# Kernel optimization log

Hardware: AMD Instinct MI355X
Metric: run time of the kernel (lower is better)

Reference implementation:

```python
import jax, jax.numpy as jnp
import numpy as np

N_NODES = 50000
N_EDGES = 500000
F_DIM = 128
N_REL = 8
N_LAYERS = 2
NEG_SLOPE = 0.2  # PyG RGATConv default negative_slope


def setup_inputs() -> dict:
    key = jax.random.key(0)
    ks = jax.random.split(key, 6)
    x = jax.random.normal(ks[0], (N_NODES, F_DIM), dtype=jnp.float32)
    edge_index = jax.random.randint(ks[1], (2, N_EDGES), 0, N_NODES)
    edge_type = jax.random.randint(ks[2], (N_EDGES,), 0, N_REL)
    # Per-layer relation weights [L, R, F_in, F_out], attention vectors q,k [L, F_out, 1], bias [L, F_out]
    W = jax.random.normal(ks[3], (N_LAYERS, N_REL, F_DIM, F_DIM), dtype=jnp.float32) * (1.0 / np.sqrt(F_DIM)).astype(np.float32)
    att_q = jax.random.normal(ks[4], (N_LAYERS, F_DIM, 1), dtype=jnp.float32) * 0.1
    att_k = jax.random.normal(ks[5], (N_LAYERS, F_DIM, 1), dtype=jnp.float32) * 0.1
    bias = jnp.zeros((N_LAYERS, F_DIM), dtype=jnp.float32)
    return {"x": x, "W": W, "att_q": att_q, "att_k": att_k, "bias": bias,
            "edge_index": edge_index, "edge_type": edge_type}


def _segment_softmax(logits, seg, num_segments):
    # Numerically stable softmax over edges grouped by destination node.
    m = jax.ops.segment_max(logits, seg, num_segments=num_segments)
    m = jax.lax.stop_gradient(m)
    e = jnp.exp(logits - m[seg])
    denom = jax.ops.segment_sum(e, seg, num_segments=num_segments)
    return e / (denom[seg] + 1e-16)


def _rgat_layer(h, src, dst, edge_type, W, q, k, b):
    # h: [N, F]; W: [R, F, F]. Project once per relation, then gather per edge
    # (avoids materializing [E, F, F] per-edge weight gathers).
    n = h.shape[0]
    xw = jnp.einsum('nf,rfg->rng', h, W)          # [R, N, F]
    out_j = xw[edge_type, src]                    # [E, F] transformed source feats
    out_i = xw[edge_type, dst]                    # [E, F] transformed dest feats
    # additive self-attention: leaky_relu(q(x_i) + k(x_j)), heads=1, dim=1
    logits = jax.nn.leaky_relu((out_i @ q + out_j @ k)[:, 0], NEG_SLOPE)  # [E]
    alpha = _segment_softmax(logits, dst, n)      # across-relation softmax per dst node
    agg = jax.ops.segment_sum(alpha[:, None] * out_j, dst, num_segments=n)  # [N, F]
    return agg + b


def reference(x, W, att_q, att_k, bias, edge_index, edge_type):
    src, dst = edge_index[0], edge_index[1]
    h = x
    for l in range(W.shape[0]):  # small fixed layer count
        h = _rgat_layer(h, src, dst, edge_type, W[l], att_q[l], att_k[l], bias[l])
        h = jax.nn.relu(h)  # dropout is identity in eval mode
    return h
```

## Files before the change

kernel.cpp:

```cpp
#include <hip/hip_runtime.h>
#include <hip/hip_bf16.h>
#include <hip/hip_fp16.h>

#define N_NODES 50000
#define N_EDGES 500000
#define F_DIM   128
#define N_REL   8
#define N_LAYERS 2
#define NEG_SLOPE 0.2f

#define NBLK_N ((N_NODES + 255) / 256)

typedef _Float16 half8 __attribute__((ext_vector_type(8)));
typedef float f32x4  __attribute__((ext_vector_type(4)));


__device__ inline float lrelu(float l) { return (l > 0.f) ? l : NEG_SLOPE * l; }

__global__ __launch_bounds__(256) void prep_h(const float* __restrict__ H,
                                              _Float16* __restrict__ Hf) {
    const size_t i8 = (size_t)blockIdx.x * 256 + threadIdx.x;
    if (i8 >= (size_t)N_NODES * F_DIM / 8) return;
    const float* src = H + i8 * 8;
    float av[8];
    *(float4*)(av)     = *(const float4*)(src);
    *(float4*)(av + 4) = *(const float4*)(src + 4);
    alignas(16) _Float16 hb[8];
#pragma unroll
    for (int j = 0; j < 8; ++j) hb[j] = (_Float16)av[j];
    *(uint4*)(Hf + i8 * 8) = *(const uint4*)hb;
}

__global__ __launch_bounds__(256) void prep_w(const float* __restrict__ W,
                                              _Float16* __restrict__ Wf) {
    __shared__ float tile[64][F_DIM + 1];
    const int mat = blockIdx.x;
    const float* src = W + (size_t)mat * F_DIM * F_DIM;
    const int t = threadIdx.x;
    for (int hf = 0; hf < 2; ++hf) {
#pragma unroll
        for (int i = 0; i < 8; ++i) {
            int idx = t + i * 256;
            int f = idx >> 5, c4 = idx & 31;
            float4 v = *(const float4*)(src + (size_t)(hf * 64 + f) * F_DIM + c4 * 4);
            *(float4*)&tile[f][c4 * 4] = v;
        }
        __syncthreads();
        int g = t >> 1, fs = (t & 1) * 32;
        for (int c = 0; c < 4; ++c) {
            alignas(16) _Float16 th[8];
#pragma unroll
            for (int j = 0; j < 8; ++j) th[j] = (_Float16)tile[fs + c * 8 + j][g];
            size_t o = ((size_t)mat * F_DIM + g) * F_DIM + hf * 64 + fs + c * 8;
            *(uint4*)(Wf + o) = *(const uint4*)th;
        }
        __syncthreads();
    }
}

#define GBM 128
#define RGRP 4
__global__ __launch_bounds__(256, 2) void gemm_xw(const _Float16* __restrict__ Hf,
                                                  const _Float16* __restrict__ Wf,
                                                  const float* __restrict__ qv_g,
                                                  const float* __restrict__ kv_g,
                                                  __half* __restrict__ xw,
                                                  float* __restrict__ a_q,
                                                  float* __restrict__ a_k) {
    __shared__ _Float16 lds[F_DIM * F_DIM];
    const int rb0 = blockIdx.x * GBM;
    const int r0  = blockIdx.y * RGRP;
    const int tid = threadIdx.x;
    const int lane = tid & 63, w = tid >> 6;
    const int q = lane >> 4, ln = lane & 15;

    half8 Af[2][4];
#pragma unroll
    for (int rt = 0; rt < 2; ++rt) {
        int row = rb0 + w * 32 + rt * 16 + ln;
        int ar = (row < N_NODES) ? row : (N_NODES - 1);
        const _Float16* hp = Hf + (size_t)ar * F_DIM;
#pragma unroll
        for (int ks = 0; ks < 4; ++ks)
            Af[rt][ks] = *(const half8*)(hp + ks * 32 + q * 8);
    }

    float qvl[8], kvl[8];
#pragma unroll
    for (int t = 0; t < 8; ++t) {
        qvl[t] = qv_g[t * 16 + ln];
        kvl[t] = kv_g[t * 16 + ln];
    }

    for (int rr = 0; rr < RGRP; ++rr) {
        const int r = r0 + rr;
        __syncthreads();
        {
            const _Float16* src = Wf + (size_t)r * F_DIM * F_DIM;
#pragma unroll
            for (int i = 0; i < 8; ++i) {
                int chunk = tid + i * 256;
                int gg = chunk >> 4, c8 = chunk & 15;
                uint4 v = *(const uint4*)(src + gg * F_DIM + c8 * 8);
                *(uint4*)(lds + gg * F_DIM + ((c8 ^ (gg & 15)) * 8)) = v;
            }
        }
        __syncthreads();

        f32x4 acc[2][8];
#pragma unroll
        for (int rt = 0; rt < 2; ++rt)
#pragma unroll
            for (int t = 0; t < 8; ++t) acc[rt][t] = (f32x4)(0.f);

#pragma unroll
        for (int ks = 0; ks < 4; ++ks) {
            const int jx = (((ks * 4 + q) ^ ln)) << 3;
            half8 Bf[8];
#pragma unroll
            for (int c = 0; c < 8; ++c)
                Bf[c] = *(const half8*)(lds + (c * 16 + ln) * F_DIM + jx);
#pragma unroll
            for (int c = 0; c < 8; ++c)
#pragma unroll
                for (int rt = 0; rt < 2; ++rt)
                    acc[rt][c] = __builtin_amdgcn_mfma_f32_16x16x32_f16(Af[rt][ks], Bf[c], acc[rt][c], 0, 0, 0);
        }

#pragma unroll
        for (int rt = 0; rt < 2; ++rt) {
            float pq[4], pk[4];
#pragma unroll
            for (int reg = 0; reg < 4; ++reg) {
                const int row = rb0 + w * 32 + rt * 16 + q * 4 + reg;
                alignas(16) unsigned short hs[8];
                float sq = 0.f, sk = 0.f;
#pragma unroll
                for (int t = 0; t < 8; ++t) {
                    float v = acc[rt][t][reg];
                    __half hv = __float2half(v);
                    hs[t] = *reinterpret_cast<unsigned short*>(&hv);
                    sq = fmaf(v, qvl[t], sq);
                    sk = fmaf(v, kvl[t], sk);
                }
                if (row < N_NODES)
                    *(uint4*)(xw + ((size_t)r * N_NODES + row) * F_DIM + ln * 8) = *(const uint4*)hs;
                pq[reg] = sq; pk[reg] = sk;
            }
#pragma unroll
            for (int reg = 0; reg < 4; ++reg) {
#pragma unroll
                for (int m = 1; m <= 8; m <<= 1) {
                    pq[reg] += __shfl_xor(pq[reg], m);
                    pk[reg] += __shfl_xor(pk[reg], m);
                }
            }
            if (ln == 0) {
#pragma unroll
                for (int reg = 0; reg < 4; ++reg) {
                    const int row = rb0 + w * 32 + rt * 16 + q * 4 + reg;
                    if (row < N_NODES) {
                        a_q[r * N_NODES + row] = pq[reg];
                        a_k[r * N_NODES + row] = pk[reg];
                    }
                }
            }
        }
    }
}


__global__ __launch_bounds__(256) void count_kernel(const int* __restrict__ dstp,
                                                    int* __restrict__ cnt) {
    int e = blockIdx.x * 256 + threadIdx.x;
    if (e < N_EDGES) atomicAdd(cnt + dstp[e], 1);
}

__global__ __launch_bounds__(256) void block_sum_kernel(const int* __restrict__ cnt,
                                                        int* __restrict__ partial) {
    __shared__ int s[256];
    int idx = blockIdx.x * 256 + threadIdx.x;
    int v = (idx < N_NODES) ? cnt[idx] : 0;
    s[threadIdx.x] = v;
    __syncthreads();
    for (int off = 128; off > 0; off >>= 1) {
        if (threadIdx.x < off) s[threadIdx.x] += s[threadIdx.x + off];
        __syncthreads();
    }
    if (threadIdx.x == 0) partial[blockIdx.x] = s[0];
}

__global__ __launch_bounds__(256) void scan_partials_kernel(int* __restrict__ partial,
                                                            int* __restrict__ row_ptr) {
    __shared__ int s[256];
    int t = threadIdx.x;
    int v = (t < NBLK_N) ? partial[t] : 0;
    s[t] = v;
    __syncthreads();
#pragma unroll
    for (int off = 1; off < 256; off <<= 1) {
        int x = (t >= off) ? s[t - off] : 0;
        __syncthreads();
        s[t] += x;
        __syncthreads();
    }
    if (t < NBLK_N) partial[t] = s[t] - v;
    if (t == 0) row_ptr[N_NODES] = N_EDGES;
}

__global__ __launch_bounds__(256) void scan_block_kernel(const int* __restrict__ cnt,
                                                         const int* __restrict__ partial,
                                                         int* __restrict__ row_ptr) {
    __shared__ int s[256];
    int t = threadIdx.x;
    int idx = blockIdx.x * 256 + t;
    int v = (idx < N_NODES) ? cnt[idx] : 0;
    s[t] = v;
    __syncthreads();
#pragma unroll
    for (int off = 1; off < 256; off <<= 1) {
        int x = (t >= off) ? s[t - off] : 0;
        __syncthreads();
        s[t] += x;
        __syncthreads();
    }
    if (idx < N_NODES) row_ptr[idx] = partial[blockIdx.x] + s[t] - v;
}

__global__ __launch_bounds__(256) void scatter_kernel(const int* __restrict__ srcp,
                                                      const int* __restrict__ dstp,
                                                      const int* __restrict__ etp,
                                                      const int* __restrict__ row_ptr,
                                                      int* __restrict__ cursor,
                                                      unsigned* __restrict__ sorted) {
    int e = blockIdx.x * 256 + threadIdx.x;
    if (e >= N_EDGES) return;
    int d = dstp[e];
    int pos = atomicAdd(cursor + d, 1);
    sorted[row_ptr[d] + pos] = (unsigned)srcp[e] | ((unsigned)etp[e] << 16);
}

__device__ inline void accum8(float* acc, uint4 v, float a) {
    const __half2* h2 = reinterpret_cast<const __half2*>(&v);
#pragma unroll
    for (int t = 0; t < 4; ++t) {
        float2 f = __half22float2(h2[t]);
        acc[t * 2]     = fmaf(a, f.x, acc[t * 2]);
        acc[t * 2 + 1] = fmaf(a, f.y, acc[t * 2 + 1]);
    }
}
__device__ inline const uint4* xwrow(const __half* xw, unsigned p, int ln) {
    return (const uint4*)(xw + (((size_t)(p >> 16)) * N_NODES + (p & 0xffff)) * F_DIM + ln * 8);
}

__global__ __launch_bounds__(256) void agg_fused(const __half* __restrict__ xw,
                                                 const float* __restrict__ a_q,
                                                 const float* __restrict__ a_k,
                                                 const int* __restrict__ row_ptr,
                                                 const unsigned* __restrict__ sorted,
                                                 const float* __restrict__ bias,
                                                 float* __restrict__ out) {
    const int lane = threadIdx.x & 63;
    const int wave = threadIdx.x >> 6;
    const int d = blockIdx.x * 4 + wave;
    if (d >= N_NODES) return;
    const int beg = row_ptr[d], end = row_ptr[d + 1];
    const int cnt = end - beg;
    const int g = lane >> 4, ln = lane & 15;

    if (cnt <= 64) {
        unsigned p = 0;
        float l = -3.4e38f;
        if (lane < cnt) {
            p = sorted[beg + lane];
            int s = p & 0xffff, t = p >> 16;
            l = lrelu(a_q[t * N_NODES + d] + a_k[t * N_NODES + s]);
        }
        float m = l;
#pragma unroll
        for (int off = 32; off > 0; off >>= 1) m = fmaxf(m, __shfl_xor(m, off));
        float ex = (lane < cnt) ? __expf(l - m) : 0.f;
        float dsum = ex;
#pragma unroll
        for (int off = 32; off > 0; off >>= 1) dsum += __shfl_xor(dsum, off);
        const float alpha = ex / (dsum + 1e-16f);

        float acc[8] = {0, 0, 0, 0, 0, 0, 0, 0};
        for (int i = 0; i < cnt; i += 8) {
            unsigned p0 = __shfl(p, i + g);
            unsigned p1 = __shfl(p, i + 4 + g);
            float a0 = __shfl(alpha, i + g);
            float a1 = __shfl(alpha, i + 4 + g);
            uint4 v0 = *xwrow(xw, p0, ln);
            uint4 v1 = *xwrow(xw, p1, ln);
            accum8(acc, v0, a0);
            accum8(acc, v1, a1);
        }
#pragma unroll
        for (int t = 0; t < 8; ++t) {
            acc[t] += __shfl_xor(acc[t], 16);
            acc[t] += __shfl_xor(acc[t], 32);
        }
        if (g == 0) {
#pragma unroll
            for (int t = 0; t < 8; ++t) {
                const int col = t * 16 + ln;
                out[(size_t)d * F_DIM + col] = fmaxf(acc[t] + bias[col], 0.f);
            }
        }
    } else {
        const int p0 = lane * 2;
        const int c0 = (p0 & 7) * 16 + (p0 >> 3);
        const int c1 = c0 + 16;
        float2 acc = make_float2(bias[c0], bias[c1]);
        float m = -3.4e38f;
        for (int i = beg + lane; i < end; i += 64) {
            unsigned p = sorted[i];
            int s = p & 0xffff, t = p >> 16;
            m = fmaxf(m, lrelu(a_q[t * N_NODES + d] + a_k[t * N_NODES + s]));
        }
#pragma unroll
        for (int off = 32; off > 0; off >>= 1) m = fmaxf(m, __shfl_xor(m, off));
        float dsum = 0.f;
        for (int i = beg + lane; i < end; i += 64) {
            unsigned p = sorted[i];
            int s = p & 0xffff, t = p >> 16;
            dsum += __expf(lrelu(a_q[t * N_NODES + d] + a_k[t * N_NODES + s]) - m);
        }
#pragma unroll
        for (int off = 32; off > 0; off >>= 1) dsum += __shfl_xor(dsum, off);
        const float inv = 1.f / (dsum + 1e-16f);
        for (int i = beg; i < end; ++i) {
            unsigned p = sorted[i];
            int s = p & 0xffff, t = p >> 16;
            float alpha = __expf(lrelu(a_q[t * N_NODES + d] + a_k[t * N_NODES + s]) - m) * inv;
            const __half2 h2 = *((const __half2*)xw + (((size_t)(p >> 16)) * N_NODES + (p & 0xffff)) * (F_DIM / 2) + lane);
            float2 v = make_float2(__half2float(h2.x), __half2float(h2.y));
            acc.x = fmaf(alpha, v.x, acc.x);
            acc.y = fmaf(alpha, v.y, acc.y);
        }
        out[(size_t)d * F_DIM + c0] = fmaxf(acc.x, 0.f);
        out[(size_t)d * F_DIM + c1] = fmaxf(acc.y, 0.f);
    }
}


extern "C" void kernel_launch(void* const* d_in, const int* in_sizes, int n_in,
                              void* d_out, int out_size, void* d_ws, size_t ws_size,
                              hipStream_t stream) {
    const float* x     = (const float*)d_in[0];
    const float* W     = (const float*)d_in[1];
    const float* att_q = (const float*)d_in[2];
    const float* att_k = (const float*)d_in[3];
    const float* bias  = (const float*)d_in[4];
    const int* ei      = (const int*)d_in[5];
    const int* etp     = (const int*)d_in[6];
    const int* srcp = ei;
    const int* dstp = ei + N_EDGES;
    float* out = (float*)d_out;
    char* ws   = (char*)d_ws;

    size_t off = 0;
    auto alloc = [&](size_t bytes) {
        void* p = ws + off;
        off = (off + bytes + 511) & ~(size_t)511;
        return p;
    };
    __half* xw       = (__half*)alloc((size_t)N_REL * N_NODES * F_DIM * sizeof(__half));
    float* a_q       = (float*)alloc((size_t)N_REL * N_NODES * sizeof(float));
    float* a_k       = (float*)alloc((size_t)N_REL * N_NODES * sizeof(float));
    int* cnt         = (int*)alloc((size_t)N_NODES * sizeof(int));
    int* row_ptr     = (int*)alloc(((size_t)N_NODES + 1) * sizeof(int));
    int* partial     = (int*)alloc(256 * sizeof(int));
    unsigned* sorted = (unsigned*)alloc((size_t)N_EDGES * sizeof(unsigned));
    _Float16* Wf     = (_Float16*)alloc((size_t)N_LAYERS * N_REL * F_DIM * F_DIM * sizeof(_Float16));
    _Float16* Hf     = (_Float16*)alloc((size_t)N_NODES * F_DIM * sizeof(_Float16));

    prep_w<<<N_LAYERS * N_REL, 256, 0, stream>>>(W, Wf);
    hipMemsetAsync(cnt, 0, (size_t)N_NODES * 4, stream);
    count_kernel<<<(N_EDGES + 255) / 256, 256, 0, stream>>>(dstp, cnt);
    block_sum_kernel<<<NBLK_N, 256, 0, stream>>>(cnt, partial);
    scan_partials_kernel<<<1, 256, 0, stream>>>(partial, row_ptr);
    scan_block_kernel<<<NBLK_N, 256, 0, stream>>>(cnt, partial, row_ptr);
    hipMemsetAsync(cnt, 0, (size_t)N_NODES * 4, stream);
    scatter_kernel<<<(N_EDGES + 255) / 256, 256, 0, stream>>>(
        srcp, dstp, etp, row_ptr, cnt, sorted);

    const int grid_h = (N_NODES * F_DIM / 8 + 255) / 256;
    const int grid_m = (N_NODES + GBM - 1) / GBM;
    for (int l = 0; l < N_LAYERS; ++l) {
        const float* H = (l == 0) ? x : out;
        prep_h<<<grid_h, 256, 0, stream>>>(H, Hf);
        gemm_xw<<<dim3(grid_m, N_REL / RGRP), 256, 0, stream>>>(
            Hf, Wf + (size_t)l * N_REL * F_DIM * F_DIM,
            att_q + l * F_DIM, att_k + l * F_DIM,
            xw, a_q, a_k);
        agg_fused<<<(N_NODES + 3) / 4, 256, 0, stream>>>(
            xw, a_q, a_k, row_ptr, sorted, bias + l * F_DIM, out);
    }
}
```

Baseline: 299.1 us.

## Fuse fp16 conversion into GEMM and skip xw rows never gathered

Removes the prep_h kernel and converts the fp32 activations to fp16 inside the GEMM's operand loads. The scatter kernel now marks which (relation, source) pairs appear in the edges, and the GEMM writes an xw row only when it is marked, cutting the large fp16 xw store traffic. The scatter also counts down from the existing counts with atomicSub, which drops one memset, and RGRP is halved from 4 to 2 to give more blocks. The cost is the added byte flag array and its memset, plus each relation group now re-reading and re-converting H.

```diff
diff --git a/kernel.cpp b/kernel.cpp
--- a/kernel.cpp
+++ b/kernel.cpp
@@ -16,20 +16,6 @@
 
 
 __device__ inline float lrelu(float l) { return (l > 0.f) ? l : NEG_SLOPE * l; }
-
-__global__ __launch_bounds__(256) void prep_h(const float* __restrict__ H,
-                                              _Float16* __restrict__ Hf) {
-    const size_t i8 = (size_t)blockIdx.x * 256 + threadIdx.x;
-    if (i8 >= (size_t)N_NODES * F_DIM / 8) return;
-    const float* src = H + i8 * 8;
-    float av[8];
-    *(float4*)(av)     = *(const float4*)(src);
-    *(float4*)(av + 4) = *(const float4*)(src + 4);
-    alignas(16) _Float16 hb[8];
-#pragma unroll
-    for (int j = 0; j < 8; ++j) hb[j] = (_Float16)av[j];
-    *(uint4*)(Hf + i8 * 8) = *(const uint4*)hb;
-}
 
 __global__ __launch_bounds__(256) void prep_w(const float* __restrict__ W,
                                               _Float16* __restrict__ Wf) {
@@ -59,11 +45,12 @@
 }
 
 #define GBM 128
-#define RGRP 4
-__global__ __launch_bounds__(256, 2) void gemm_xw(const _Float16* __restrict__ Hf,
+#define RGRP 2
+__global__ __launch_bounds__(256, 2) void gemm_xw(const float* __restrict__ H,
                                                   const _Float16* __restrict__ Wf,
                                                   const float* __restrict__ qv_g,
                                                   const float* __restrict__ kv_g,
+                                                  const unsigned char* __restrict__ used,
                                                   __half* __restrict__ xw,
                                                   float* __restrict__ a_q,
                                                   float* __restrict__ a_k) {
@@ -79,10 +66,17 @@
     for (int rt = 0; rt < 2; ++rt) {
         int row = rb0 + w * 32 + rt * 16 + ln;
         int ar = (row < N_NODES) ? row : (N_NODES - 1);
-        const _Float16* hp = Hf + (size_t)ar * F_DIM;
-#pragma unroll
-        for (int ks = 0; ks < 4; ++ks)
-            Af[rt][ks] = *(const half8*)(hp + ks * 32 + q * 8);
+        const float* hp = H + (size_t)ar * F_DIM;
+#pragma unroll
+        for (int ks = 0; ks < 4; ++ks) {
+            float av[8];
+            *(float4*)(av)     = *(const float4*)(hp + ks * 32 + q * 8);
+            *(float4*)(av + 4) = *(const float4*)(hp + ks * 32 + q * 8 + 4);
+            half8 h;
+#pragma unroll
+            for (int j = 0; j < 8; ++j) h[j] = (_Float16)av[j];
+            Af[rt][ks] = h;
+        }
     }
 
     float qvl[8], kvl[8];
@@ -143,7 +137,7 @@
                     sq = fmaf(v, qvl[t], sq);
                     sk = fmaf(v, kvl[t], sk);
                 }
-                if (row < N_NODES)
+                if (row < N_NODES && used[(size_t)r * N_NODES + row])
                     *(uint4*)(xw + ((size_t)r * N_NODES + row) * F_DIM + ln * 8) = *(const uint4*)hs;
                 pq[reg] = sq; pk[reg] = sk;
             }
@@ -231,13 +225,15 @@
                                                       const int* __restrict__ dstp,
                                                       const int* __restrict__ etp,
                                                       const int* __restrict__ row_ptr,
-                                                      int* __restrict__ cursor,
-                                                      unsigned* __restrict__ sorted) {
+                                                      int* __restrict__ cnt,
+                                                      unsigned* __restrict__ sorted,
+                                                      unsigned char* __restrict__ used) {
     int e = blockIdx.x * 256 + threadIdx.x;
     if (e >= N_EDGES) return;
-    int d = dstp[e];
-    int pos = atomicAdd(cursor + d, 1);
-    sorted[row_ptr[d] + pos] = (unsigned)srcp[e] | ((unsigned)etp[e] << 16);
+    int d = dstp[e], s = srcp[e], t = etp[e];
+    int pos = atomicSub(cnt + d, 1) - 1;
+    sorted[row_ptr[d] + pos] = (unsigned)s | ((unsigned)t << 16);
+    used[(size_t)t * N_NODES + s] = 1;
 }
 
 __device__ inline void accum8(float* acc, uint4 v, float a) {
@@ -369,31 +365,32 @@
     __half* xw       = (__half*)alloc((size_t)N_REL * N_NODES * F_DIM * sizeof(__half));
     float* a_q       = (float*)alloc((size_t)N_REL * N_NODES * sizeof(float));
     float* a_k       = (float*)alloc((size_t)N_REL * N_NODES * sizeof(float));
-    int* cnt         = (int*)alloc((size_t)N_NODES * sizeof(int));
+    const size_t cnt_bytes  = (size_t)N_NODES * sizeof(int);
+    const size_t cnt_pad    = (cnt_bytes + 511) & ~(size_t)511;
+    const size_t used_bytes = (size_t)N_REL * N_NODES;
+    char* zeroblk    = (char*)alloc(cnt_pad + used_bytes);
+    int* cnt         = (int*)zeroblk;
+    unsigned char* used = (unsigned char*)(zeroblk + cnt_pad);
     int* row_ptr     = (int*)alloc(((size_t)N_NODES + 1) * sizeof(int));
     int* partial     = (int*)alloc(256 * sizeof(int));
     unsigned* sorted = (unsigned*)alloc((size_t)N_EDGES * sizeof(unsigned));
     _Float16* Wf     = (_Float16*)alloc((size_t)N_LAYERS * N_REL * F_DIM * F_DIM * sizeof(_Float16));
-    _Float16* Hf     = (_Float16*)alloc((size_t)N_NODES * F_DIM * sizeof(_Float16));
 
     prep_w<<<N_LAYERS * N_REL, 256, 0, stream>>>(W, Wf);
-    hipMemsetAsync(cnt, 0, (size_t)N_NODES * 4, stream);
+    hipMemsetAsync(zeroblk, 0, cnt_pad + used_bytes, stream);
     count_kernel<<<(N_EDGES + 255) / 256, 256, 0, stream>>>(dstp, cnt);
     block_sum_kernel<<<NBLK_N, 256, 0, stream>>>(cnt, partial);
     scan_partials_kernel<<<1, 256, 0, stream>>>(partial, row_ptr);
     scan_block_kernel<<<NBLK_N, 256, 0, stream>>>(cnt, partial, row_ptr);
-    hipMemsetAsync(cnt, 0, (size_t)N_NODES * 4, stream);
     scatter_kernel<<<(N_EDGES + 255) / 256, 256, 0, stream>>>(
-        srcp, dstp, etp, row_ptr, cnt, sorted);
-
-    const int grid_h = (N_NODES * F_DIM / 8 + 255) / 256;
+        srcp, dstp, etp, row_ptr, cnt, sorted, used);
+
     const int grid_m = (N_NODES + GBM - 1) / GBM;
     for (int l = 0; l < N_LAYERS; ++l) {
         const float* H = (l == 0) ? x : out;
-        prep_h<<<grid_h, 256, 0, stream>>>(H, Hf);
         gemm_xw<<<dim3(grid_m, N_REL / RGRP), 256, 0, stream>>>(
-            Hf, Wf + (size_t)l * N_REL * F_DIM * F_DIM,
-            att_q + l * F_DIM, att_k + l * F_DIM,
+            H, Wf + (size_t)l * N_REL * F_DIM * F_DIM,
+            att_q + l * F_DIM, att_k + l * F_DIM, used,
             xw, a_q, a_k);
         agg_fused<<<(N_NODES + 3) / 4, 256, 0, stream>>>(
             xw, a_q, a_k, row_ptr, sorted, bias + l * F_DIM, out);
```

Result: no change. 299.4 us (+0.1%).
